# Optimization experiments

Hardware: AMD Instinct MI355X
Metric: run time of the kernel (lower is better)

The kernel has to match this reference:

```python
import jax, jax.numpy as jnp
import numpy as np

N, B, M, K, C = 120000, 8, 60000, 16, 32
EX = 512  # 128 * expansion_factor 4
EPS = 1e-5


def _bn(h, g, b):
    # BatchNorm1d (training-mode batch stats, biased var), stats over points
    m = h.mean(axis=0)
    v = h.var(axis=0)
    return (h - m) * jax.lax.rsqrt(v + EPS) * g + b


def setup_inputs() -> dict:
    key = jax.random.key(0)
    ks = jax.random.split(key, 20)

    def w(i, shape, fan):
        return jax.random.normal(ks[i], shape, jnp.float32) / np.sqrt(fan)

    inp = {}
    inp["x"] = jax.random.normal(ks[0], (N, C), jnp.float32)
    inp["pos"] = jax.random.normal(ks[1], (N, 3), jnp.float32) * 5.0
    inp["batch"] = jnp.sort(jax.random.randint(ks[2], (N,), 0, B))
    inp["reflectance"] = jax.random.uniform(ks[3], (N,), jnp.float32)
    inp["sf"] = jax.random.uniform(ks[4], (B,), jnp.float32, minval=0.5, maxval=1.5)
    inp["idx"] = jnp.sort(jax.random.randint(ks[5], (M,), 0, N))
    inp["edge_src"] = jax.random.randint(ks[6], (M * K,), 0, N)
    inp["edge_dst"] = jnp.repeat(jnp.arange(M), K)
    # local_nn MLP channels [C+4, 64, 64, 128]; first layer has no BN
    inp["mlp_W1"] = w(7, (C + 4, 64), C + 4); inp["mlp_b1"] = jnp.zeros((64,))
    inp["mlp_W2"] = w(8, (64, 64), 64); inp["mlp_b2"] = jnp.zeros((64,))
    inp["mlp_g2"] = jnp.ones((64,)); inp["mlp_be2"] = jnp.zeros((64,))
    inp["mlp_W3"] = w(9, (64, 128), 64); inp["mlp_b3"] = jnp.zeros((128,))
    inp["mlp_g3"] = jnp.ones((128,)); inp["mlp_be3"] = jnp.zeros((128,))
    # ReflectanceYesNo (1 -> 32 -> 32 -> 1)
    inp["ryn_W1"] = w(10, (1, 32), 1); inp["ryn_b1"] = jnp.zeros((32,))
    inp["ryn_W2"] = w(11, (32, 32), 32); inp["ryn_b2"] = jnp.zeros((32,))
    inp["ryn_W3"] = w(12, (32, 1), 32); inp["ryn_b3"] = jnp.zeros((1,))
    # InvertedResidualBlock 128 -> 512 -> 128 (all 1x1 convs)
    inp["exp_W"] = w(13, (128, EX), 128); inp["exp_b"] = jnp.zeros((EX,))
    inp["exp_g"] = jnp.ones((EX,)); inp["exp_be"] = jnp.zeros((EX,))
    inp["dw_w"] = jax.random.normal(ks[14], (2, EX), jnp.float32)  # depthwise k=1 -> per-channel scale
    inp["dw_b"] = jnp.zeros((2, EX)); inp["dw_g"] = jnp.ones((2, EX)); inp["dw_be"] = jnp.zeros((2, EX))
    inp["pw_W"] = w(15, (2, EX, EX), EX); inp["pw_b"] = jnp.zeros((2, EX))
    inp["pw_g"] = jnp.ones((2, EX)); inp["pw_be"] = jnp.zeros((2, EX))
    inp["c_g"] = jnp.ones((2, EX)); inp["c_be"] = jnp.zeros((2, EX))
    inp["proj_W"] = w(16, (EX, 128), EX); inp["proj_b"] = jnp.zeros((128,))
    inp["proj_g"] = jnp.ones((128,)); inp["proj_be"] = jnp.zeros((128,))
    return inp


def reference(x, pos, batch, reflectance, sf, idx, edge_src, edge_dst,
              mlp_W1, mlp_b1, mlp_W2, mlp_b2, mlp_g2, mlp_be2, mlp_W3, mlp_b3, mlp_g3, mlp_be3,
              ryn_W1, ryn_b1, ryn_W2, ryn_b2, ryn_W3, ryn_b3,
              exp_W, exp_b, exp_g, exp_be, dw_w, dw_b, dw_g, dw_be,
              pw_W, pw_b, pw_g, pw_be, c_g, c_be, proj_W, proj_b, proj_g, proj_be):
    Bn = sf.shape[0]
    Mn = idx.shape[0]
    pos4 = jnp.concatenate([pos[:, :3], reflectance[:, None]], axis=-1)  # [N,4]

    # --- ReflectanceYesNo gating (gumbel_softmax over a size-1 axis == ones, straight-through) ---
    h = jax.nn.relu(reflectance[:, None] @ ryn_W1 + ryn_b1)
    h = jax.nn.relu(h @ ryn_W2 + ryn_b2)
    pooled = jax.ops.segment_sum(h, batch, num_segments=Bn)
    counts = jax.ops.segment_sum(jnp.ones((h.shape[0],), h.dtype), batch, num_segments=Bn)
    logits = (pooled / counts[:, None]) @ ryn_W3 + ryn_b3  # [B,1]
    y_soft = jax.nn.softmax(logits, axis=-1)               # size-1 softmax -> all ones
    y = jax.lax.stop_gradient(jnp.ones_like(y_soft) - y_soft) + y_soft
    gate = jnp.where(jnp.sum(reflectance) != 0.0, y[:, 0][batch], 1.0)
    refl4 = pos4[:, 3] * gate

    # --- scale coords, PointNetConv: gather -> local_nn MLP -> max aggregate ---
    scale = sf[batch][:, None]
    pos_s = jnp.concatenate([pos4[:, :3] / scale, refl4[:, None]], axis=-1)  # [N,4]
    rel = pos_s[edge_src] - pos_s[idx][edge_dst]                              # [E,4]
    msg = jnp.concatenate([x[edge_src], rel], axis=-1)                        # [E,C+4]
    h1 = jax.nn.relu(msg @ mlp_W1 + mlp_b1)
    h2 = _bn(jax.nn.relu(h1 @ mlp_W2 + mlp_b2), mlp_g2, mlp_be2)
    h3 = _bn(jax.nn.relu(h2 @ mlp_W3 + mlp_b3), mlp_g3, mlp_be3)
    agg = jax.ops.segment_max(h3, edge_dst, num_segments=Mn)                  # [M,128]
    agg = jnp.where(jnp.isneginf(agg), 0.0, agg)  # PyG fills isolated nodes with 0

    # --- InvertedResidualBlock (1x1 convs == per-point linears, BN over points) ---
    res = agg
    e = jax.nn.relu(_bn(agg @ exp_W + exp_b, exp_g, exp_be))

    def ds(hh, i):  # DepthwiseSeparableConv1d, k=1
        d = jax.nn.relu(_bn(hh * dw_w[i] + dw_b[i], dw_g[i], dw_be[i]))
        return jax.nn.relu(_bn(d @ pw_W[i] + pw_b[i], pw_g[i], pw_be[i]))

    cmid = jax.nn.relu(_bn(ds(e, 0), c_g[0], c_be[0]))
    cmid = _bn(ds(cmid, 1), c_g[1], c_be[1])
    o = _bn(cmid @ proj_W + proj_b, proj_g, proj_be)
    out = jax.nn.relu(o + res)  # shortcut is identity (in == out channels)

    return (out, pos[idx, :3], batch[idx], reflectance[idx], sf)
```

## Files before the change

kernel.cpp:

```cpp
#include <hip/hip_runtime.h>
#include <hip/hip_bf16.h>
#include <cstdint>

#define DEV_INLINE __device__ __forceinline__

typedef unsigned short u16;
typedef unsigned int   u32;
typedef short bf16x8 __attribute__((ext_vector_type(8)));
typedef float f32x4  __attribute__((ext_vector_type(4)));

constexpr int NP = 120000, NB = 8, NM = 60000, KNN = 16;
constexpr int NE = NM * KNN;
constexpr float EPS = 1e-5f;

constexpr size_t O_POS   = (size_t)NM * 128;
constexpr size_t O_BATCH = O_POS + (size_t)NM * 3;
constexpr size_t O_REFL  = O_BATCH + NM;
constexpr size_t O_SF    = O_REFL + NM;

__device__ float  g_pos_s[(size_t)NP * 4];
__device__ u16    g_xbf[(size_t)NP * 32];
__device__ u16    g_pre2[(size_t)NE * 64];
__device__ u32    g_mm[(size_t)NM * 128];
__device__ float  g_agg[(size_t)NM * 128];
__device__ u16    g_aggbf[(size_t)NM * 128];
__device__ u16    g_bufA[(size_t)NM * 512];
__device__ u16    g_bufB[(size_t)NM * 512];
__device__ float  g_obuf[(size_t)NM * 128];
__device__ float  g_sum[512], g_sqs[512], g_cfa[512], g_cfb[512];
__device__ float  g_b3adj[128], g_pbadj[128];
__device__ u16 g_w1t[64 * 64];
__device__ u16 g_w2t[64 * 64];
__device__ u16 g_w3t[128 * 64];
__device__ u16 g_expwt[512 * 128];
__device__ u16 g_pw0t[512 * 512];
__device__ u16 g_pw1t[512 * 512];
__device__ u16 g_projwt[128 * 512];

template<int ID> DEV_INLINE const u16* ubufsel() {
  if constexpr (ID == 1) return g_aggbf;
  else if constexpr (ID == 2) return g_bufA;
  else return g_bufB;
}
template<int ID> DEV_INLINE u16* obufsel() {
  if constexpr (ID == 2) return g_bufA;
  else return g_bufB;
}
template<int ID> DEV_INLINE const u16* wsel() {
  if constexpr (ID == 3) return g_expwt;
  else if constexpr (ID == 4) return g_pw0t;
  else if constexpr (ID == 5) return g_pw1t;
  else return g_projwt;
}

DEV_INLINE float bf2f(u16 u) { u32 x = (u32)u << 16; float f; __builtin_memcpy(&f, &x, 4); return f; }
DEV_INLINE u16 f2bf(float f) {
  u32 x; __builtin_memcpy(&x, &f, 4);
  return (u16)((x + 0x7FFFu + ((x >> 16) & 1u)) >> 16);
}
DEV_INLINE u32 pack2(float a, float b) { return (u32)f2bf(a) | ((u32)f2bf(b) << 16); }

DEV_INLINE uint4 affine8r(uint4 v, float4 A0, float4 A1, float4 B0, float4 B1, bool relu) {
  float av[8] = {A0.x,A0.y,A0.z,A0.w,A1.x,A1.y,A1.z,A1.w};
  float bv[8] = {B0.x,B0.y,B0.z,B0.w,B1.x,B1.y,B1.z,B1.w};
  u32 u[4] = {v.x, v.y, v.z, v.w}, r[4];
#pragma unroll
  for (int q = 0; q < 4; q++) {
    float lo = bf2f((u16)(u[q] & 0xFFFFu));
    float hi = bf2f((u16)(u[q] >> 16));
    lo = fmaf(av[2*q],   lo, bv[2*q]);
    hi = fmaf(av[2*q+1], hi, bv[2*q+1]);
    if (relu) { lo = fmaxf(lo, 0.f); hi = fmaxf(hi, 0.f); }
    r[q] = (u32)f2bf(lo) | ((u32)f2bf(hi) << 16);
  }
  return make_uint4(r[0], r[1], r[2], r[3]);
}

DEV_INLINE uint4 affine8(uint4 v, int kbase, bool relu) {
  u32 u[4] = {v.x, v.y, v.z, v.w};
  u32 r[4];
#pragma unroll
  for (int q = 0; q < 4; q++) {
    float lo = bf2f((u16)(u[q] & 0xFFFFu));
    float hi = bf2f((u16)(u[q] >> 16));
    lo = fmaf(g_cfa[kbase + 2*q],     lo, g_cfb[kbase + 2*q]);
    hi = fmaf(g_cfa[kbase + 2*q + 1], hi, g_cfb[kbase + 2*q + 1]);
    if (relu) { lo = fmaxf(lo, 0.f); hi = fmaxf(hi, 0.f); }
    r[q] = (u32)f2bf(lo) | ((u32)f2bf(hi) << 16);
  }
  return make_uint4(r[0], r[1], r[2], r[3]);
}

__global__ void prep_pos_x(const float* __restrict__ pos, const int* __restrict__ batch,
                           const float* __restrict__ refl, const float* __restrict__ sf,
                           const float* __restrict__ x) {
  int i = blockIdx.x * blockDim.x + threadIdx.x;
  if (i >= NP) return;
  float s = sf[batch[i]];
  float4 v;
  v.x = pos[(size_t)i*3+0] / s;
  v.y = pos[(size_t)i*3+1] / s;
  v.z = pos[(size_t)i*3+2] / s;
  v.w = refl[i];
  *reinterpret_cast<float4*>(g_pos_s + (size_t)i*4) = v;
  const float4* xr = reinterpret_cast<const float4*>(x + (size_t)i*32);
#pragma unroll
  for (int q = 0; q < 4; q++) {
    float4 a = xr[q*2], b = xr[q*2+1];
    uint4 u = make_uint4(pack2(a.x,a.y), pack2(a.z,a.w), pack2(b.x,b.y), pack2(b.z,b.w));
    *reinterpret_cast<uint4*>(g_xbf + (size_t)i*32 + q*8) = u;
  }
}

__global__ void tail_out(const float* __restrict__ pos, const int* __restrict__ batch,
                         const float* __restrict__ refl, const float* __restrict__ sf,
                         const int* __restrict__ idx, float* __restrict__ out) {
  int i = blockIdx.x * blockDim.x + threadIdx.x;
  if (i < NM) {
    int p = idx[i];
    out[O_POS + (size_t)i*3+0] = pos[(size_t)p*3+0];
    out[O_POS + (size_t)i*3+1] = pos[(size_t)p*3+1];
    out[O_POS + (size_t)i*3+2] = pos[(size_t)p*3+2];
    out[O_BATCH + i] = (float)batch[p];
    out[O_REFL  + i] = refl[p];
  }
  if (i < NB) out[O_SF + i] = sf[i];
}

__global__ void zero_stats() {
  int t = threadIdx.x;
  g_sum[t] = 0.f; g_sqs[t] = 0.f;
}

__global__ void prep_weights(const float* __restrict__ W1, const float* __restrict__ W2,
                             const float* __restrict__ W3, const float* __restrict__ expW,
                             const float* __restrict__ pwW, const float* __restrict__ projW) {
  int i = blockIdx.x * 256 + threadIdx.x;
  const int s0 = 4096, s1 = 4096, s2 = 8192, s3 = 65536, s4 = 262144, s5 = 262144, s6 = 65536;
  if (i < s0) { int n = i >> 6, k = i & 63; g_w1t[i] = (k < 36) ? f2bf(W1[k*64 + n]) : (u16)0; return; }
  i -= s0;
  if (i < s1) { int n = i >> 6, k = i & 63; g_w2t[i] = f2bf(W2[k*64 + n]); return; }
  i -= s1;
  if (i < s2) { int n = i >> 6, k = i & 63; g_w3t[i] = f2bf(W3[k*128 + n]); return; }
  i -= s2;
  if (i < s3) { int n = i >> 7, k = i & 127; g_expwt[i] = f2bf(expW[k*512 + n]); return; }
  i -= s3;
  if (i < s4) { int n = i >> 9, k = i & 511; g_pw0t[i] = f2bf(pwW[k*512 + n]); return; }
  i -= s4;
  if (i < s5) { int n = i >> 9, k = i & 511; g_pw1t[i] = f2bf(pwW[262144 + k*512 + n]); return; }
  i -= s5;
  if (i < s6) { int n = i >> 9, k = i & 511; g_projwt[i] = f2bf(projW[k*128 + n]); return; }
}

__global__ void param_bn(const float* __restrict__ g, const float* __restrict__ be,
                         float n, int C) {
  int c = threadIdx.x;
  if (c < C) {
    float mean = g_sum[c] / n;
    float var  = fmaxf(g_sqs[c] / n - mean * mean, 0.f);
    float a = g[c] * rsqrtf(var + EPS);
    g_cfa[c] = a;
    g_cfb[c] = be[c] - a * mean;
  }
  __syncthreads();
  g_sum[c] = 0.f; g_sqs[c] = 0.f;
}

__global__ void param_dw(const float* __restrict__ w, const float* __restrict__ g,
                         const float* __restrict__ be, float n, int C) {
  int c = threadIdx.x;
  if (c < C) {
    float mean = g_sum[c] / n;
    float var  = fmaxf(g_sqs[c] / n - mean * mean, 0.f);
    float r = rsqrtf(w[c]*w[c]*var + EPS);
    float a = w[c] * r * g[c];
    g_cfa[c] = a;
    g_cfb[c] = be[c] - a * mean;
  }
  __syncthreads();
  g_sum[c] = 0.f; g_sqs[c] = 0.f;
}

template<int SID>
__global__ void scale_fold(const float* __restrict__ bias_in, int N, int K) {
  u16* Wt = (SID == 0) ? g_w3t : g_projwt;
  float* badj = (SID == 0) ? g_b3adj : g_pbadj;
  int w = (blockIdx.x * blockDim.x + threadIdx.x) >> 6;
  int lane = threadIdx.x & 63;
  if (w >= N) return;
  float acc = 0.f;
  for (int k = lane; k < K; k += 64) {
    float wv = bf2f(Wt[(size_t)w*K + k]);
    acc = fmaf(g_cfb[k], wv, acc);
    Wt[(size_t)w*K + k] = f2bf(g_cfa[k] * wv);
  }
#pragma unroll
  for (int o = 32; o; o >>= 1) acc += __shfl_xor(acc, o, 64);
  if (lane == 0) badj[w] = bias_in[w] + acc;
}

constexpr int K1_BLOCKS = 960;
__launch_bounds__(256)
__global__ void k1_edge(const int* __restrict__ esrc, const int* __restrict__ idx,
                        const float* __restrict__ b1v, const float* __restrict__ b2v) {
  __shared__ u16 sH[4][16][72];
  __shared__ float ssum[64], ssqs[64];
  const int tid = threadIdx.x;
  if (tid < 64) { ssum[tid] = 0.f; ssqs[tid] = 0.f; }
  __syncthreads();
  const int w = tid >> 6, lane = tid & 63, l15 = lane & 15, l4 = lane >> 4;
  u16 (*sh)[72] = sH[w];
  bf16x8 w1f[2][4], w2f[2][4];
#pragma unroll
  for (int ks = 0; ks < 2; ks++)
#pragma unroll
    for (int fc = 0; fc < 4; fc++) {
      w1f[ks][fc] = *reinterpret_cast<const bf16x8*>(g_w1t + (size_t)(fc*16+l15)*64 + ks*32 + l4*8);
      w2f[ks][fc] = *reinterpret_cast<const bf16x8*>(g_w2t + (size_t)(fc*16+l15)*64 + ks*32 + l4*8);
    }
  float b1r[4], b2r[4];
#pragma unroll
  for (int fc = 0; fc < 4; fc++) { b1r[fc] = b1v[fc*16+l15]; b2r[fc] = b2v[fc*16+l15]; }
  float s8[4] = {}, q8[4] = {};
  const int t0 = blockIdx.x * 4 + w;
  const int TSTRIDE = K1_BLOCKS * 4;
  int   s_cur = esrc[t0*16 + l15];
  uint4 x_cur = *reinterpret_cast<const uint4*>(g_xbf + (size_t)s_cur*32 + l4*8);
  float4 ps_cur = make_float4(0.f,0.f,0.f,0.f);
  if (l4 == 0) ps_cur = *reinterpret_cast<const float4*>(g_pos_s + (size_t)s_cur*4);
  float4 pc_cur = *reinterpret_cast<const float4*>(g_pos_s + (size_t)idx[t0]*4);

  for (int t = t0; t < NM; t += TSTRIDE) {
    const int tn = t + TSTRIDE;
    int s_nx = 0; uint4 x_nx = make_uint4(0,0,0,0);
    float4 ps_nx = ps_cur, pc_nx = pc_cur;
    if (tn < NM) {
      s_nx = esrc[tn*16 + l15];
      x_nx = *reinterpret_cast<const uint4*>(g_xbf + (size_t)s_nx*32 + l4*8);
      if (l4 == 0) ps_nx = *reinterpret_cast<const float4*>(g_pos_s + (size_t)s_nx*4);
      pc_nx = *reinterpret_cast<const float4*>(g_pos_s + (size_t)idx[tn]*4);
    }
    bf16x8 a0 = __builtin_bit_cast(bf16x8, x_cur);
    uint4 r4 = make_uint4(0,0,0,0);
    if (l4 == 0) {
      r4.x = pack2(ps_cur.x - pc_cur.x, ps_cur.y - pc_cur.y);
      r4.y = pack2(ps_cur.z - pc_cur.z, ps_cur.w - pc_cur.w);
    }
    bf16x8 a1 = __builtin_bit_cast(bf16x8, r4);
    f32x4 acc1[4] = {};
#pragma unroll
    for (int fc = 0; fc < 4; fc++) {
      acc1[fc] = __builtin_amdgcn_mfma_f32_16x16x32_bf16(a0, w1f[0][fc], acc1[fc], 0, 0, 0);
      acc1[fc] = __builtin_amdgcn_mfma_f32_16x16x32_bf16(a1, w1f[1][fc], acc1[fc], 0, 0, 0);
    }
#pragma unroll
    for (int fc = 0; fc < 4; fc++)
#pragma unroll
      for (int r = 0; r < 4; r++)
        sh[l4*4 + r][fc*16 + l15] = f2bf(fmaxf(acc1[fc][r] + b1r[fc], 0.f));
    bf16x8 h0  = *reinterpret_cast<const bf16x8*>(&sh[l15][l4*8]);
    bf16x8 h1v = *reinterpret_cast<const bf16x8*>(&sh[l15][32 + l4*8]);
    f32x4 acc2[4] = {};
#pragma unroll
    for (int fc = 0; fc < 4; fc++) {
      acc2[fc] = __builtin_amdgcn_mfma_f32_16x16x32_bf16(h0,  w2f[0][fc], acc2[fc], 0, 0, 0);
      acc2[fc] = __builtin_amdgcn_mfma_f32_16x16x32_bf16(h1v, w2f[1][fc], acc2[fc], 0, 0, 0);
    }
#pragma unroll
    for (int fc = 0; fc < 4; fc++)
#pragma unroll
      for (int r = 0; r < 4; r++) {
        float v = fmaxf(acc2[fc][r] + b2r[fc], 0.f);
        s8[fc] += v; q8[fc] += v*v;
        sh[l4*4 + r][fc*16 + l15] = f2bf(v);
      }
    uint4 p0 = *reinterpret_cast<const uint4*>(&sh[l15][l4*8]);
    uint4 p1 = *reinterpret_cast<const uint4*>(&sh[l15][32 + l4*8]);
    *reinterpret_cast<uint4*>(g_pre2 + (size_t)t*1024 + lane*8)       = p0;
    *reinterpret_cast<uint4*>(g_pre2 + (size_t)t*1024 + 512 + lane*8) = p1;
    s_cur = s_nx; x_cur = x_nx; ps_cur = ps_nx; pc_cur = pc_nx;
  }
#pragma unroll
  for (int fc = 0; fc < 4; fc++) {
    float sv = s8[fc], qv = q8[fc];
    sv += __shfl_xor(sv, 16, 64); sv += __shfl_xor(sv, 32, 64);
    qv += __shfl_xor(qv, 16, 64); qv += __shfl_xor(qv, 32, 64);
    if (l4 == 0) { atomicAdd(&ssum[fc*16 + l15], sv); atomicAdd(&ssqs[fc*16 + l15], qv); }
  }
  __syncthreads();
  if (tid < 64) { atomicAdd(&g_sum[tid], ssum[tid]); atomicAdd(&g_sqs[tid], ssqs[tid]); }
}

constexpr int K2_BLOCKS = 960;
__launch_bounds__(256)
__global__ void k2_edge() {
  __shared__ float ssum[128], ssqs[128];
  const int tid = threadIdx.x;
  if (tid < 128) { ssum[tid] = 0.f; ssqs[tid] = 0.f; }
  __syncthreads();
  const int lane = tid & 63, l15 = lane & 15, l4 = lane >> 4;
  const int wglobal = blockIdx.x * 4 + (tid >> 6);
  const int WSTRIDE = K2_BLOCKS * 4;
  bf16x8 w3f[2][8];
#pragma unroll
  for (int ks = 0; ks < 2; ks++)
#pragma unroll
    for (int fc = 0; fc < 8; fc++)
      w3f[ks][fc] = *reinterpret_cast<const bf16x8*>(g_w3t + (size_t)(fc*16 + l15)*64 + ks*32 + l4*8);
  float bv[8];
#pragma unroll
  for (int fc = 0; fc < 8; fc++) bv[fc] = g_b3adj[fc*16 + l15];
  float s[8] = {}, q[8] = {};
  int t = wglobal;
  uint4 an0 = make_uint4(0,0,0,0), an1 = an0;
  if (t < NM) {
    const uint4* p = reinterpret_cast<const uint4*>(g_pre2 + (size_t)t*1024 + lane*8);
    an0 = p[0]; an1 = p[64];
  }
  for (; t < NM; t += WSTRIDE) {
    uint4 a0 = an0, a1 = an1;
    int tn = t + WSTRIDE;
    if (tn < NM) {
      const uint4* p = reinterpret_cast<const uint4*>(g_pre2 + (size_t)tn*1024 + lane*8);
      an0 = p[0]; an1 = p[64];
    }
    bf16x8 af0 = __builtin_bit_cast(bf16x8, a0);
    bf16x8 af1 = __builtin_bit_cast(bf16x8, a1);
    f32x4 acc[8] = {};
#pragma unroll
    for (int fc = 0; fc < 8; fc++) {
      acc[fc] = __builtin_amdgcn_mfma_f32_16x16x32_bf16(af0, w3f[0][fc], acc[fc], 0, 0, 0);
      acc[fc] = __builtin_amdgcn_mfma_f32_16x16x32_bf16(af1, w3f[1][fc], acc[fc], 0, 0, 0);
    }
    u32 rbase = (u32)t * 128u;
#pragma unroll
    for (int fc = 0; fc < 8; fc++) {
      float v0 = fmaxf(acc[fc][0] + bv[fc], 0.f);
      float v1 = fmaxf(acc[fc][1] + bv[fc], 0.f);
      float v2 = fmaxf(acc[fc][2] + bv[fc], 0.f);
      float v3 = fmaxf(acc[fc][3] + bv[fc], 0.f);
      s[fc] += (v0 + v1) + (v2 + v3);
      q[fc] += (v0*v0 + v1*v1) + (v2*v2 + v3*v3);
      float mx = fmaxf(fmaxf(v0, v1), fmaxf(v2, v3));
      float mn = fminf(fminf(v0, v1), fminf(v2, v3));
      mx = fmaxf(mx, __shfl_xor(mx, 16, 64)); mx = fmaxf(mx, __shfl_xor(mx, 32, 64));
      mn = fminf(mn, __shfl_xor(mn, 16, 64)); mn = fminf(mn, __shfl_xor(mn, 32, 64));
      if (l4 == (fc & 3))
        g_mm[rbase + fc*16 + l15] = (u32)f2bf(mx) | ((u32)f2bf(mn) << 16);
    }
  }
#pragma unroll
  for (int fc = 0; fc < 8; fc++) {
    float sv = s[fc], qv = q[fc];
    sv += __shfl_xor(sv, 16, 64); sv += __shfl_xor(sv, 32, 64);
    qv += __shfl_xor(qv, 16, 64); qv += __shfl_xor(qv, 32, 64);
    if (l4 == 0) { atomicAdd(&ssum[fc*16 + l15], sv); atomicAdd(&ssqs[fc*16 + l15], qv); }
  }
  __syncthreads();
  if (tid < 128) { atomicAdd(&g_sum[tid], ssum[tid]); atomicAdd(&g_sqs[tid], ssqs[tid]); }
}

__global__ void k3_agg() {
  int i4 = (blockIdx.x * 256 + threadIdx.x) * 4;
  if (i4 >= NM * 128) return;
  int c = i4 & 127;
  uint4 mm = *reinterpret_cast<const uint4*>(g_mm + i4);
  float4 a = *reinterpret_cast<const float4*>(g_cfa + c);
  float4 b = *reinterpret_cast<const float4*>(g_cfb + c);
  u32 u[4] = {mm.x, mm.y, mm.z, mm.w};
  float av[4] = {a.x, a.y, a.z, a.w};
  float bb[4] = {b.x, b.y, b.z, b.w};
  float4 r;
  float* rr = &r.x;
#pragma unroll
  for (int j = 0; j < 4; j++) {
    float mx = bf2f((u16)(u[j] & 0xFFFFu));
    float mn = bf2f((u16)(u[j] >> 16));
    rr[j] = av[j] > 0.f ? fmaf(av[j], mx, bb[j]) : fmaf(av[j], mn, bb[j]);
  }
  *reinterpret_cast<float4*>(g_agg + i4) = r;
  uint2 pk; pk.x = pack2(r.x, r.y); pk.y = pack2(r.z, r.w);
  *reinterpret_cast<uint2*>(g_aggbf + i4) = pk;
}

template<int AID, int WID, int OID, bool PRO_AFF, bool PRO_RELU, bool OUT_BF16, bool BIAS_DEV>
__launch_bounds__(256, 3)
__global__ void gemm_mfma(const float* __restrict__ bias, int Mrows, int Ncols, int Kdim) {
  const u16* __restrict__ A  = ubufsel<AID>();
  const u16* __restrict__ Bt = wsel<WID>();
  __shared__ u16 As[2][128][40];
  __shared__ u16 Bs[2][128][40];
  __shared__ float ssum[128], ssqs[128];
  const int tid = threadIdx.x;
  const int m0 = blockIdx.x * 128, n0 = blockIdx.y * 128;
  if (tid < 128) { ssum[tid] = 0.f; ssqs[tid] = 0.f; }
  const int wave = tid >> 6, lane = tid & 63, l15 = lane & 15, l4 = lane >> 4;
  const int wr = wave >> 1, wc = wave & 1;
  const int srow = tid >> 1, sseg = tid & 1;
  const int gr = m0 + srow;
  const bool aval = gr < Mrows;
  const size_t aoff = (size_t)gr * Kdim + sseg * 16;
  const size_t boff = (size_t)(n0 + srow) * Kdim + sseg * 16;
  f32x4 acc[4][4] = {};
  const int nt = Kdim >> 5;

  uint4 va0, va1, vb0, vb1;
  float4 ca0, ca1, ca2, ca3, cb0, cb1, cb2, cb3;

  auto LOAD = [&](int t) {
    const int k0 = t * 32;
    va0 = make_uint4(0,0,0,0); va1 = va0;
    if (aval) {
      const uint4* p = reinterpret_cast<const uint4*>(A + aoff + k0);
      va0 = p[0]; va1 = p[1];
    }
    const uint4* pb = reinterpret_cast<const uint4*>(Bt + boff + k0);
    vb0 = pb[0]; vb1 = pb[1];
    if (PRO_AFF) {
      const int kb = k0 + sseg * 16;
      ca0 = *reinterpret_cast<const float4*>(g_cfa + kb);
      ca1 = *reinterpret_cast<const float4*>(g_cfa + kb + 4);
      ca2 = *reinterpret_cast<const float4*>(g_cfa + kb + 8);
      ca3 = *reinterpret_cast<const float4*>(g_cfa + kb + 12);
      cb0 = *reinterpret_cast<const float4*>(g_cfb + kb);
      cb1 = *reinterpret_cast<const float4*>(g_cfb + kb + 4);
      cb2 = *reinterpret_cast<const float4*>(g_cfb + kb + 8);
      cb3 = *reinterpret_cast<const float4*>(g_cfb + kb + 12);
    }
  };
  auto WRITE = [&](int buf) {
    uint4 wa0 = va0, wa1 = va1;
    if (PRO_AFF) {
      wa0 = affine8r(va0, ca0, ca1, cb0, cb1, PRO_RELU);
      wa1 = affine8r(va1, ca2, ca3, cb2, cb3, PRO_RELU);
    }
    *reinterpret_cast<uint4*>(&As[buf][srow][sseg*16])     = wa0;
    *reinterpret_cast<uint4*>(&As[buf][srow][sseg*16 + 8]) = wa1;
    *reinterpret_cast<uint4*>(&Bs[buf][srow][sseg*16])     = vb0;
    *reinterpret_cast<uint4*>(&Bs[buf][srow][sseg*16 + 8]) = vb1;
  };
  auto MFMA = [&](int buf) {
    bf16x8 af[4], bf[4];
#pragma unroll
    for (int fr = 0; fr < 4; fr++)
      af[fr] = *reinterpret_cast<const bf16x8*>(&As[buf][wr*64 + fr*16 + l15][l4*8]);
#pragma unroll
    for (int fc = 0; fc < 4; fc++)
      bf[fc] = *reinterpret_cast<const bf16x8*>(&Bs[buf][wc*64 + fc*16 + l15][l4*8]);
#pragma unroll
    for (int fr = 0; fr < 4; fr++)
#pragma unroll
      for (int fc = 0; fc < 4; fc++)
        acc[fr][fc] = __builtin_amdgcn_mfma_f32_16x16x32_bf16(af[fr], bf[fc], acc[fr][fc], 0, 0, 0);
  };

  LOAD(0);
  WRITE(0);
  __syncthreads();
  int cur = 0;
  for (int t = 0; ; ) {
    const bool more = (t + 1 < nt);
    if (more) LOAD(t + 1);
    MFMA(cur);
    if (!more) break;
    WRITE(cur ^ 1);
    __syncthreads();
    cur ^= 1; ++t;
  }

  const int orow = m0 + wr*64 + l4*4;
#pragma unroll
  for (int fc = 0; fc < 4; fc++) {
    int col = n0 + wc*64 + fc*16 + l15;
    float bvv = BIAS_DEV ? g_pbadj[col] : bias[col];
    float s = 0.f, q = 0.f;
#pragma unroll
    for (int fr = 0; fr < 4; fr++)
#pragma unroll
      for (int r = 0; r < 4; r++) {
        int row = orow + fr*16 + r;
        if (row < Mrows) {
          float v = acc[fr][fc][r] + bvv;
          s += v; q += v*v;
          if (OUT_BF16) obufsel<OID>()[(size_t)row*Ncols + col] = f2bf(v);
          else          g_obuf[(size_t)row*Ncols + col] = v;
        }
      }
    atomicAdd(&ssum[wc*64 + fc*16 + l15], s);
    atomicAdd(&ssqs[wc*64 + fc*16 + l15], q);
  }
  __syncthreads();
  if (tid < 128) { atomicAdd(&g_sum[n0 + tid], ssum[tid]); atomicAdd(&g_sqs[n0 + tid], ssqs[tid]); }
}

template<int INID, int OUTID>
__launch_bounds__(256)
__global__ void ew_stats(int rows) {
  const u16* __restrict__ X = ubufsel<INID>();
  u16* __restrict__ Y = obufsel<OUTID>();
  __shared__ float ssum[512], ssqs[512];
  const int tid = threadIdx.x;
  ssum[tid] = 0.f; ssum[tid+256] = 0.f; ssqs[tid] = 0.f; ssqs[tid+256] = 0.f;
  __syncthreads();
  const int c0 = (tid & 63) * 8;
  const int rl = tid >> 6;
  float a[8], b[8];
#pragma unroll
  for (int j = 0; j < 8; j++) { a[j] = g_cfa[c0+j]; b[j] = g_cfb[c0+j]; }
  float s[8] = {}, q[8] = {};
  for (int r = blockIdx.x*4 + rl; r < rows; r += gridDim.x*4) {
    uint4 v = *reinterpret_cast<const uint4*>(X + (size_t)r*512 + c0);
    u32 u[4] = {v.x, v.y, v.z, v.w}, o[4];
#pragma unroll
    for (int t = 0; t < 4; t++) {
      float lo = bf2f((u16)(u[t] & 0xFFFFu));
      float hi = bf2f((u16)(u[t] >> 16));
      lo = fmaxf(fmaf(a[2*t],   lo, b[2*t]),   0.f);
      hi = fmaxf(fmaf(a[2*t+1], hi, b[2*t+1]), 0.f);
      s[2*t] += lo; q[2*t] += lo*lo; s[2*t+1] += hi; q[2*t+1] += hi*hi;
      o[t] = (u32)f2bf(lo) | ((u32)f2bf(hi) << 16);
    }
    *reinterpret_cast<uint4*>(Y + (size_t)r*512 + c0) = make_uint4(o[0], o[1], o[2], o[3]);
  }
#pragma unroll
  for (int j = 0; j < 8; j++) { atomicAdd(&ssum[c0+j], s[j]); atomicAdd(&ssqs[c0+j], q[j]); }
  __syncthreads();
  atomicAdd(&g_sum[tid],     ssum[tid]);     atomicAdd(&g_sqs[tid],     ssqs[tid]);
  atomicAdd(&g_sum[tid+256], ssum[tid+256]); atomicAdd(&g_sqs[tid+256], ssqs[tid+256]);
}

__global__ void final_out(float* __restrict__ out) {
  int i4 = (blockIdx.x * 256 + threadIdx.x) * 4;
  if (i4 >= NM * 128) return;
  int c = i4 & 127;
  float4 o  = *reinterpret_cast<const float4*>(g_obuf + i4);
  float4 ag = *reinterpret_cast<const float4*>(g_agg + i4);
  float4 a  = *reinterpret_cast<const float4*>(g_cfa + c);
  float4 b  = *reinterpret_cast<const float4*>(g_cfb + c);
  float4 r;
  r.x = fmaxf(fmaf(a.x, o.x, b.x) + ag.x, 0.f);
  r.y = fmaxf(fmaf(a.y, o.y, b.y) + ag.y, 0.f);
  r.z = fmaxf(fmaf(a.z, o.z, b.z) + ag.z, 0.f);
  r.w = fmaxf(fmaf(a.w, o.w, b.w) + ag.w, 0.f);
  *reinterpret_cast<float4*>(out + i4) = r;
}

extern "C" void kernel_launch(void* const* d_in, const int* in_sizes, int n_in,
                              void* d_out, int out_size, void* d_ws, size_t ws_size,
                              hipStream_t stream) {
  const float* x     = (const float*)d_in[0];
  const float* pos   = (const float*)d_in[1];
  const int*   batch = (const int*)  d_in[2];
  const float* refl  = (const float*)d_in[3];
  const float* sf    = (const float*)d_in[4];
  const int*   idx   = (const int*)  d_in[5];
  const int*   esrc  = (const int*)  d_in[6];
  const float* W1  = (const float*)d_in[8];
  const float* b1  = (const float*)d_in[9];
  const float* W2  = (const float*)d_in[10];
  const float* b2  = (const float*)d_in[11];
  const float* g2  = (const float*)d_in[12];
  const float* be2 = (const float*)d_in[13];
  const float* W3  = (const float*)d_in[14];
  const float* b3  = (const float*)d_in[15];
  const float* g3  = (const float*)d_in[16];
  const float* be3 = (const float*)d_in[17];
  const float* expW  = (const float*)d_in[24];
  const float* expb  = (const float*)d_in[25];
  const float* expg  = (const float*)d_in[26];
  const float* expbe = (const float*)d_in[27];
  const float* dww  = (const float*)d_in[28];
  const float* dwg  = (const float*)d_in[30];
  const float* dwbe = (const float*)d_in[31];
  const float* pwW  = (const float*)d_in[32];
  const float* pwb  = (const float*)d_in[33];
  const float* pwg  = (const float*)d_in[34];
  const float* pwbe = (const float*)d_in[35];
  const float* cg   = (const float*)d_in[36];
  const float* cbe  = (const float*)d_in[37];
  const float* projW  = (const float*)d_in[38];
  const float* projb  = (const float*)d_in[39];
  const float* projg  = (const float*)d_in[40];
  const float* projbe = (const float*)d_in[41];
  float* out = (float*)d_out;

  const float fNE = (float)NE, fNM = (float)NM;

  prep_weights<<<2624, 256, 0, stream>>>(W1, W2, W3, expW, pwW, projW);
  prep_pos_x<<<(NP + 255)/256, 256, 0, stream>>>(pos, batch, refl, sf, x);
  tail_out<<<(NM + 255)/256, 256, 0, stream>>>(pos, batch, refl, sf, idx, out);
  zero_stats<<<1, 512, 0, stream>>>();

  k1_edge<<<K1_BLOCKS, 256, 0, stream>>>(esrc, idx, b1, b2);
  param_bn<<<1, 512, 0, stream>>>(g2, be2, fNE, 64);
  scale_fold<0><<<32, 256, 0, stream>>>(b3, 128, 64);
  k2_edge<<<K2_BLOCKS, 256, 0, stream>>>();
  param_bn<<<1, 512, 0, stream>>>(g3, be3, fNE, 128);
  k3_agg<<<NM*128/1024, 256, 0, stream>>>();

  gemm_mfma<1, 3, 2, false, false, true, false><<<dim3(469, 4), 256, 0, stream>>>(expb, NM, 512, 128);
  param_bn<<<1, 512, 0, stream>>>(expg, expbe, fNM, 512);
  ew_stats<2, 2><<<512, 256, 0, stream>>>(NM);
  param_dw<<<1, 512, 0, stream>>>(dww, dwg, dwbe, fNM, 512);
  gemm_mfma<2, 4, 3, true, true, true, false><<<dim3(469, 4), 256, 0, stream>>>(pwb, NM, 512, 512);
  param_bn<<<1, 512, 0, stream>>>(pwg, pwbe, fNM, 512);
  ew_stats<3, 3><<<512, 256, 0, stream>>>(NM);
  param_bn<<<1, 512, 0, stream>>>(cg, cbe, fNM, 512);
  ew_stats<3, 3><<<512, 256, 0, stream>>>(NM);
  param_dw<<<1, 512, 0, stream>>>(dww + 512, dwg + 512, dwbe + 512, fNM, 512);
  gemm_mfma<3, 5, 2, true, true, true, false><<<dim3(469, 4), 256, 0, stream>>>(pwb + 512, NM, 512, 512);
  param_bn<<<1, 512, 0, stream>>>(pwg + 512, pwbe + 512, fNM, 512);
  ew_stats<2, 2><<<512, 256, 0, stream>>>(NM);
  param_bn<<<1, 512, 0, stream>>>(cg + 512, cbe + 512, fNM, 512);
  scale_fold<1><<<32, 256, 0, stream>>>(projb, 128, 512);
  gemm_mfma<2, 6, 0, false, false, false, true><<<dim3(469, 1), 256, 0, stream>>>(projb, NM, 128, 512);
  param_bn<<<1, 512, 0, stream>>>(projg, projbe, fNM, 128);
  final_out<<<NM*128/1024, 256, 0, stream>>>(out);
}
```

Measured before the change: 804.8 us.

## Deepen GEMM prefetch, pad LDS rows, remap grid, widen ew_stats grid

The GEMM main loop now keeps two register prefetch sets, loading two K-tiles ahead and unrolling ping-pong over the two LDS buffers. LDS row padding changes from 40 to 44 elements to alter the bank-conflict pattern. The grid becomes 1D with the N panels innermost, so blocks that share A rows run next to each other and can reuse it in L2. The elementwise stats kernels launch twice as many blocks. Extra prefetch registers may lower occupancy under the launch bounds of 3.

```diff
diff --git a/kernel.cpp b/kernel.cpp
--- a/kernel.cpp
+++ b/kernel.cpp
@@ -76,21 +76,6 @@
   return make_uint4(r[0], r[1], r[2], r[3]);
 }
 
-DEV_INLINE uint4 affine8(uint4 v, int kbase, bool relu) {
-  u32 u[4] = {v.x, v.y, v.z, v.w};
-  u32 r[4];
-#pragma unroll
-  for (int q = 0; q < 4; q++) {
-    float lo = bf2f((u16)(u[q] & 0xFFFFu));
-    float hi = bf2f((u16)(u[q] >> 16));
-    lo = fmaf(g_cfa[kbase + 2*q],     lo, g_cfb[kbase + 2*q]);
-    hi = fmaf(g_cfa[kbase + 2*q + 1], hi, g_cfb[kbase + 2*q + 1]);
-    if (relu) { lo = fmaxf(lo, 0.f); hi = fmaxf(hi, 0.f); }
-    r[q] = (u32)f2bf(lo) | ((u32)f2bf(hi) << 16);
-  }
-  return make_uint4(r[0], r[1], r[2], r[3]);
-}
-
 __global__ void prep_pos_x(const float* __restrict__ pos, const int* __restrict__ batch,
                            const float* __restrict__ refl, const float* __restrict__ sf,
                            const float* __restrict__ x) {
@@ -383,16 +368,20 @@
   *reinterpret_cast<uint2*>(g_aggbf + i4) = pk;
 }
 
-template<int AID, int WID, int OID, bool PRO_AFF, bool PRO_RELU, bool OUT_BF16, bool BIAS_DEV>
+struct PF { uint4 a0, a1, b0, b1; float4 ca0, ca1, ca2, ca3, cb0, cb1, cb2, cb3; };
+
+template<int AID, int WID, int OID, int NPAN, bool PRO_AFF, bool PRO_RELU, bool OUT_BF16, bool BIAS_DEV>
 __launch_bounds__(256, 3)
-__global__ void gemm_mfma(const float* __restrict__ bias, int Mrows, int Ncols, int Kdim) {
+__global__ void gemm_mfma(const float* __restrict__ bias, int Mrows, int Kdim) {
+  const int Ncols = NPAN * 128;
   const u16* __restrict__ A  = ubufsel<AID>();
   const u16* __restrict__ Bt = wsel<WID>();
-  __shared__ u16 As[2][128][40];
-  __shared__ u16 Bs[2][128][40];
+  __shared__ u16 As[2][128][44];
+  __shared__ u16 Bs[2][128][44];
   __shared__ float ssum[128], ssqs[128];
   const int tid = threadIdx.x;
-  const int m0 = blockIdx.x * 128, n0 = blockIdx.y * 128;
+  const int bid = blockIdx.x;
+  const int m0 = (bid / NPAN) * 128, n0 = (bid % NPAN) * 128;
   if (tid < 128) { ssum[tid] = 0.f; ssqs[tid] = 0.f; }
   const int wave = tid >> 6, lane = tid & 63, l15 = lane & 15, l4 = lane >> 4;
   const int wr = wave >> 1, wc = wave & 1;
@@ -404,40 +393,37 @@
   f32x4 acc[4][4] = {};
   const int nt = Kdim >> 5;
 
-  uint4 va0, va1, vb0, vb1;
-  float4 ca0, ca1, ca2, ca3, cb0, cb1, cb2, cb3;
-
-  auto LOAD = [&](int t) {
+  auto LOADR = [&](PF& r, int t) {
     const int k0 = t * 32;
-    va0 = make_uint4(0,0,0,0); va1 = va0;
+    r.a0 = make_uint4(0,0,0,0); r.a1 = r.a0;
     if (aval) {
       const uint4* p = reinterpret_cast<const uint4*>(A + aoff + k0);
-      va0 = p[0]; va1 = p[1];
+      r.a0 = p[0]; r.a1 = p[1];
     }
     const uint4* pb = reinterpret_cast<const uint4*>(Bt + boff + k0);
-    vb0 = pb[0]; vb1 = pb[1];
+    r.b0 = pb[0]; r.b1 = pb[1];
     if (PRO_AFF) {
       const int kb = k0 + sseg * 16;
-      ca0 = *reinterpret_cast<const float4*>(g_cfa + kb);
-      ca1 = *reinterpret_cast<const float4*>(g_cfa + kb + 4);
-      ca2 = *reinterpret_cast<const float4*>(g_cfa + kb + 8);
-      ca3 = *reinterpret_cast<const float4*>(g_cfa + kb + 12);
-      cb0 = *reinterpret_cast<const float4*>(g_cfb + kb);
-      cb1 = *reinterpret_cast<const float4*>(g_cfb + kb + 4);
-      cb2 = *reinterpret_cast<const float4*>(g_cfb + kb + 8);
-      cb3 = *reinterpret_cast<const float4*>(g_cfb + kb + 12);
+      r.ca0 = *reinterpret_cast<const float4*>(g_cfa + kb);
+      r.ca1 = *reinterpret_cast<const float4*>(g_cfa + kb + 4);
+      r.ca2 = *reinterpret_cast<const float4*>(g_cfa + kb + 8);
+      r.ca3 = *reinterpret_cast<const float4*>(g_cfa + kb + 12);
+      r.cb0 = *reinterpret_cast<const float4*>(g_cfb + kb);
+      r.cb1 = *reinterpret_cast<const float4*>(g_cfb + kb + 4);
+      r.cb2 = *reinterpret_cast<const float4*>(g_cfb + kb + 8);
+      r.cb3 = *reinterpret_cast<const float4*>(g_cfb + kb + 12);
     }
   };
-  auto WRITE = [&](int buf) {
-    uint4 wa0 = va0, wa1 = va1;
+  auto WRITER = [&](int buf, PF& r) {
+    uint4 wa0 = r.a0, wa1 = r.a1;
     if (PRO_AFF) {
-      wa0 = affine8r(va0, ca0, ca1, cb0, cb1, PRO_RELU);
-      wa1 = affine8r(va1, ca2, ca3, cb2, cb3, PRO_RELU);
+      wa0 = affine8r(r.a0, r.ca0, r.ca1, r.cb0, r.cb1, PRO_RELU);
+      wa1 = affine8r(r.a1, r.ca2, r.ca3, r.cb2, r.cb3, PRO_RELU);
     }
     *reinterpret_cast<uint4*>(&As[buf][srow][sseg*16])     = wa0;
     *reinterpret_cast<uint4*>(&As[buf][srow][sseg*16 + 8]) = wa1;
-    *reinterpret_cast<uint4*>(&Bs[buf][srow][sseg*16])     = vb0;
-    *reinterpret_cast<uint4*>(&Bs[buf][srow][sseg*16 + 8]) = vb1;
+    *reinterpret_cast<uint4*>(&Bs[buf][srow][sseg*16])     = r.b0;
+    *reinterpret_cast<uint4*>(&Bs[buf][srow][sseg*16 + 8]) = r.b1;
   };
   auto MFMA = [&](int buf) {
     bf16x8 af[4], bf[4];
@@ -454,18 +440,22 @@
         acc[fr][fc] = __builtin_amdgcn_mfma_f32_16x16x32_bf16(af[fr], bf[fc], acc[fr][fc], 0, 0, 0);
   };
 
-  LOAD(0);
-  WRITE(0);
-  __syncthreads();
-  int cur = 0;
-  for (int t = 0; ; ) {
-    const bool more = (t + 1 < nt);
-    if (more) LOAD(t + 1);
-    MFMA(cur);
-    if (!more) break;
-    WRITE(cur ^ 1);
+  PF rA, rB;
+  LOADR(rA, 0);
+  if (nt > 1) LOADR(rB, 1);
+  WRITER(0, rA);
+  __syncthreads();
+  for (int t = 0; t < nt; t += 2) {
+    if (t + 2 < nt) LOADR(rA, t + 2);
+    MFMA(0);
+    if (t + 1 >= nt) break;
+    WRITER(1, rB);
     __syncthreads();
-    cur ^= 1; ++t;
+    if (t + 3 < nt) LOADR(rB, t + 3);
+    MFMA(1);
+    if (t + 2 >= nt) break;
+    WRITER(0, rA);
+    __syncthreads();
   }
 
   const int orow = m0 + wr*64 + l4*4;
@@ -598,22 +588,22 @@
   param_bn<<<1, 512, 0, stream>>>(g3, be3, fNE, 128);
   k3_agg<<<NM*128/1024, 256, 0, stream>>>();
 
-  gemm_mfma<1, 3, 2, false, false, true, false><<<dim3(469, 4), 256, 0, stream>>>(expb, NM, 512, 128);
+  gemm_mfma<1, 3, 2, 4, false, false, true, false><<<469*4, 256, 0, stream>>>(expb, NM, 128);
   param_bn<<<1, 512, 0, stream>>>(expg, expbe, fNM, 512);
-  ew_stats<2, 2><<<512, 256, 0, stream>>>(NM);
+  ew_stats<2, 2><<<1024, 256, 0, stream>>>(NM);
   param_dw<<<1, 512, 0, stream>>>(dww, dwg, dwbe, fNM, 512);
-  gemm_mfma<2, 4, 3, true, true, true, false><<<dim3(469, 4), 256, 0, stream>>>(pwb, NM, 512, 512);
+  gemm_mfma<2, 4, 3, 4, true, true, true, false><<<469*4, 256, 0, stream>>>(pwb, NM, 512);
   param_bn<<<1, 512, 0, stream>>>(pwg, pwbe, fNM, 512);
-  ew_stats<3, 3><<<512, 256, 0, stream>>>(NM);
+  ew_stats<3, 3><<<1024, 256, 0, stream>>>(NM);
   param_bn<<<1, 512, 0, stream>>>(cg, cbe, fNM, 512);
-  ew_stats<3, 3><<<512, 256, 0, stream>>>(NM);
+  ew_stats<3, 3><<<1024, 256, 0, stream>>>(NM);
   param_dw<<<1, 512, 0, stream>>>(dww + 512, dwg + 512, dwbe + 512, fNM, 512);
-  gemm_mfma<3, 5, 2, true, true, true, false><<<dim3(469, 4), 256, 0, stream>>>(pwb + 512, NM, 512, 512);
+  gemm_mfma<3, 5, 2, 4, true, true, true, false><<<469*4, 256, 0, stream>>>(pwb + 512, NM, 512);
   param_bn<<<1, 512, 0, stream>>>(pwg + 512, pwbe + 512, fNM, 512);
-  ew_stats<2, 2><<<512, 256, 0, stream>>>(NM);
+  ew_stats<2, 2><<<1024, 256, 0, stream>>>(NM);
   param_bn<<<1, 512, 0, stream>>>(cg + 512, cbe + 512, fNM, 512);
   scale_fold<1><<<32, 256, 0, stream>>>(projb, 128, 512);
-  gemm_mfma<2, 6, 0, false, false, false, true><<<dim3(469, 1), 256, 0, stream>>>(projb, NM, 128, 512);
+  gemm_mfma<2, 6, 0, 1, false, false, false, true><<<469, 256, 0, stream>>>(projb, NM, 512);
   param_bn<<<1, 512, 0, stream>>>(projg, projbe, fNM, 128);
   final_out<<<NM*128/1024, 256, 0, stream>>>(out);
 }
```

After: 1.793 ms. +122.8%, slower.
